# Kernel optimization log

Measured on AMD Instinct MI355X. Metric: run time of the kernel, lower is better.

## Reference

```python
import jax, jax.numpy as jnp
import numpy as np

IOU_THRESHOLDS = (0.5, 0.75)
B, N, G = 256, 4000, 50


def _iou(amin, amax, bmin, bmax):
    # broadcasted temporal IoU: anchors [N,1] vs boxes [1,G] -> [N,G]
    inter = jnp.maximum(jnp.minimum(amax, bmax) - jnp.maximum(amin, bmin), 0.0)
    union = (amax - amin) + (bmax - bmin) - inter
    return inter / union


def _greedy_tp(segments, gts, thr):
    # segments: [N,2], gts: [G,2]. Replicates AP.get_values greedy matching:
    # for each label (in order), claim the first (lowest-index) unused proposal
    # whose IoU > thr. Final used-mask == is_TP.
    ious = _iou(segments[:, 0:1], segments[:, 1:2], gts[None, :, 0], gts[None, :, 1])  # [N,G]
    pot = ious > thr
    n = segments.shape[0]

    def step(used, col):  # col: [N] bool, candidates for this label
        cand = col & ~used
        idx = jnp.argmax(cand)  # first True (argmax of bool is first max)
        used = jnp.where(jnp.any(cand), used.at[idx].set(True), used)
        return used, None

    used, _ = jax.lax.scan(step, jnp.zeros((n,), jnp.bool_), pot.T)
    return used  # [N] bool


def _ap_for_threshold(scores, segments, labels, thr):
    is_tp = jax.vmap(lambda s, g: _greedy_tp(s, g, thr))(segments, labels)  # [B,N]
    conf = scores.reshape(-1)                       # [B*N]
    tp = is_tp.reshape(-1).astype(jnp.float32)
    order = jnp.argsort(-conf)                      # sort by confidence, descending
    tp = tp[order]
    n_labels = labels.shape[0] * labels.shape[1]
    m = tp.shape[0]
    acc_tp = jnp.cumsum(tp)
    precision = acc_tp / (jnp.arange(m, dtype=jnp.float32) + 1.0)
    recall = acc_tp / jnp.float32(n_labels)
    # curve = [[1,0]] then (recall, precision) reversed; AP = sum(|dx| * cummax(y)[:-1])
    x = jnp.concatenate([jnp.ones((1,), jnp.float32), recall[::-1]])
    y = jnp.concatenate([jnp.zeros((1,), jnp.float32), precision[::-1]])
    y_max = jax.lax.cummax(y, axis=0)
    x_diff = jnp.abs(jnp.diff(x))
    return jnp.sum(x_diff * y_max[:-1])


def setup_inputs() -> dict:
    key = jax.random.key(0)
    k1, k2, k3, k4, k5 = jax.random.split(key, 5)
    scores = jax.random.uniform(k1, (B, N), dtype=jnp.float32)
    p_start = jax.random.uniform(k2, (B, N), dtype=jnp.float32) * 0.9
    p_len = jax.random.uniform(k3, (B, N), dtype=jnp.float32) * 0.1 + 0.005
    segments = jnp.stack([p_start, p_start + p_len], axis=-1)  # [B,N,2], start<end
    g_start = jax.random.uniform(k4, (B, G), dtype=jnp.float32) * 0.9
    g_len = jax.random.uniform(k5, (B, G), dtype=jnp.float32) * 0.1 + 0.005
    labels = jnp.stack([g_start, g_start + g_len], axis=-1)    # [B,G,2]
    return {"scores": scores, "segments": segments, "labels": labels}


def reference(scores, segments, labels):
    # returns AP at each IoU threshold, shape [len(IOU_THRESHOLDS)]
    return jnp.stack([_ap_for_threshold(scores, segments, labels, t) for t in IOU_THRESHOLDS])
```

## Files before the change

### kernel.cpp

```cpp
#include <hip/hip_runtime.h>


#define B_ 256
#define N_ 4000
#define G_ 50
#define M_ (B_ * N_)
#define NL_ (B_ * G_)
#define NBKT 1024
#define KP 16
#define TILE (NL_ / KP)

#define M0_ 0x1.000001p-1
#define M1_ 0x1.800001p-1

typedef unsigned long long u64;

__device__ __forceinline__ unsigned bucket_of(float c) {
    unsigned b = (unsigned)(c * 1024.0f);
    return b > (NBKT - 1) ? (NBKT - 1) : b;
}

__global__ __launch_bounds__(1024) void tp_kernel(
    const float* __restrict__ seg,
    const float* __restrict__ gts,
    const float* __restrict__ conf,
    int* __restrict__ tpIdx,
    int* __restrict__ cnt,
    unsigned short* __restrict__ pbh)
{
    const int tid  = threadIdx.x;
    const int lane = tid & 63;
    const int wv   = tid >> 6;
    const int b    = blockIdx.x;

    __shared__ float2 gtl[G_];
    __shared__ u64 cand[2][G_][64];
    __shared__ unsigned hls[NBKT];
    __shared__ int lcnt[2];

    if (tid < NBKT) hls[tid] = 0u;
    if (tid < G_) gtl[tid] = ((const float2*)gts)[b * G_ + tid];
    if (tid < 2) lcnt[tid] = 0;
    __syncthreads();

    const float* cb = conf + (size_t)b * N_;
    #pragma unroll
    for (int s = 0; s < 4; ++s) {
        int n = s * 1024 + tid;
        if (n < N_) atomicAdd(&hls[bucket_of(cb[n])], 1u);
    }

    const float2* sb = (const float2*)(seg + (size_t)b * (N_ * 2));
    float pmin[4], pmax[4], plen[4];
    #pragma unroll
    for (int s = 0; s < 4; ++s) {
        int n = s * 1024 + tid;
        if (n < N_) { float2 v = sb[n]; pmin[s] = v.x; pmax[s] = v.y; }
        else { pmin[s] = 1e9f; pmax[s] = 1e9f; }
        plen[s] = pmax[s] - pmin[s];
    }
    for (int g = 0; g < G_; ++g) {
        float2 gt = gtl[g];
        float glen = gt.y - gt.x;
        u64 m0[4], m1[4];
        #pragma unroll
        for (int s = 0; s < 4; ++s) {
            float inter = fmaxf(fminf(pmax[s], gt.y) - fmaxf(pmin[s], gt.x), 0.0f);
            float uni = plen[s] + glen - inter;
            double di = (double)inter;
            double du = (double)uni;
            m0[s] = __ballot(di > M0_ * du);
            m1[s] = __ballot(di > M1_ * du);
        }
        if (lane == 0) {
            #pragma unroll
            for (int s = 0; s < 4; ++s) {
                cand[0][g][s * 16 + wv] = m0[s];
                cand[1][g][s * 16 + wv] = m1[s];
            }
        }
    }
    __syncthreads();

    if (tid < NBKT) pbh[(size_t)b * NBKT + tid] = (unsigned short)hls[tid];

    if (wv < 2) {
        const int thr_i = wv;
        u64 used = 0ull;
        for (int g = 0; g < G_; ++g) {
            u64 c = cand[thr_i][g][lane] & ~used;
            u64 ball = __ballot(c != 0ull);
            if (ball) {
                int fl = __ffsll(ball) - 1;
                if (lane == fl) used |= (c & (0ull - c));
            }
        }
        int cpop = __popcll(used);
        if (cpop) {
            int j = atomicAdd(&lcnt[thr_i], cpop);
            u64 u = used;
            while (u) {
                int bit = __ffsll(u) - 1;
                u &= u - 1;
                tpIdx[thr_i * NL_ + b * G_ + j++] = b * N_ + lane * 64 + bit;
            }
        }
    }
    __syncthreads();
    if (tid < 2) cnt[tid * B_ + b] = lcnt[tid];
}

__global__ __launch_bounds__(256) void s1_kernel(
    unsigned short* __restrict__ pbh,
    unsigned* __restrict__ total)
{
    __shared__ unsigned sc[256];
    const int bin = blockIdx.x;
    const int b = threadIdx.x;
    unsigned v = pbh[(size_t)b * NBKT + bin];
    sc[b] = v;
    __syncthreads();
    for (int off = 1; off < 256; off <<= 1) {
        unsigned add = (b >= off) ? sc[b - off] : 0u;
        __syncthreads();
        sc[b] += add;
        __syncthreads();
    }
    pbh[(size_t)b * NBKT + bin] = (unsigned short)(sc[b] - v);
    if (b == 255) total[bin] = sc[255];
}

__global__ __launch_bounds__(1024) void s2_kernel(
    const unsigned* __restrict__ total, unsigned* __restrict__ binStart)
{
    __shared__ unsigned part[1024];
    int t = threadIdx.x;
    part[t] = total[t];
    __syncthreads();
    for (int off = 1; off < 1024; off <<= 1) {
        unsigned add = (t >= off) ? part[t - off] : 0u;
        __syncthreads();
        part[t] += add;
        __syncthreads();
    }
    binStart[t] = (t == 0) ? 0u : part[t - 1];
}

__global__ __launch_bounds__(1024) void scatter_kernel(
    const float* __restrict__ conf,
    const unsigned short* __restrict__ pbh,
    const unsigned* __restrict__ binStart,
    u64* __restrict__ sKey)
{
    __shared__ unsigned baseB[NBKT];
    __shared__ unsigned lofs[NBKT];
    const int tid = threadIdx.x;
    const int b = blockIdx.x;
    if (tid < NBKT) {
        baseB[tid] = binStart[tid] + pbh[(size_t)b * NBKT + tid];
        lofs[tid] = 0u;
    }
    __syncthreads();
    const float* cb = conf + (size_t)b * N_;
    #pragma unroll
    for (int s = 0; s < 4; ++s) {
        int n = s * 1024 + tid;
        if (n < N_) {
            float c = cb[n];
            unsigned bin = bucket_of(c);
            unsigned lo = atomicAdd(&lofs[bin], 1u);
            unsigned idx = (unsigned)(b * N_ + n);
            sKey[baseB[bin] + lo] = ((u64)__float_as_uint(c) << 32) | (u64)(0xFFFFFFFFu - idx);
        }
    }
}

__global__ __launch_bounds__(256) void rank_kernel(
    const float* __restrict__ conf,
    const int* __restrict__ tpIdx,
    const int* __restrict__ cnt,
    const unsigned* __restrict__ total,
    const unsigned* __restrict__ binStart,
    const u64* __restrict__ sKey,
    int* __restrict__ tpRank)
{
    const int lane = threadIdx.x & 63;
    const int w = (blockIdx.x << 2) | (threadIdx.x >> 6);
    if (w >= 2 * NL_) return;
    const int thr_i = w / NL_;
    const int t = w - thr_i * NL_;
    const int batch = t / G_;
    const int j = t - batch * G_;

    if (j < cnt[thr_i * B_ + batch]) {
        int e = tpIdx[thr_i * NL_ + t];
        float c = conf[e];
        u64 keyE = ((u64)__float_as_uint(c) << 32) | (u64)(0xFFFFFFFFu - (unsigned)e);
        unsigned bin = bucket_of(c);
        unsigned lo = binStart[bin], n = total[bin];
        int r = M_ - (int)lo - (int)n;
        for (unsigned base = 0; base < n; base += 64) {
            unsigned k = base + lane;
            bool pred = (k < n) && (sKey[lo + k] > keyE);
            r += (int)__popcll(__ballot(pred));
        }
        if (lane == 0) tpRank[thr_i * NL_ + t] = r;
    } else {
        if (lane == 0) tpRank[thr_i * NL_ + t] = M_ + t;
    }
}

__global__ __launch_bounds__(256) void pos1_kernel(
    const int* __restrict__ tpRank,
    int* __restrict__ pcount)
{
    __shared__ alignas(16) int tile[TILE];
    const int k = blockIdx.y, thr_i = blockIdx.z;
    const int* base = tpRank + thr_i * NL_;
    for (int i = threadIdx.x; i < TILE; i += 256)
        tile[i] = base[k * TILE + i];
    __syncthreads();

    const int t0 = blockIdx.x * 1024 + threadIdx.x;
    int r[4], c[4] = {0, 0, 0, 0};
    #pragma unroll
    for (int j = 0; j < 4; ++j) {
        int t = t0 + j * 256;
        r[j] = (t < NL_) ? base[t] : -1;
    }
    const int4* l4 = (const int4*)tile;
    #pragma unroll 4
    for (int i = 0; i < TILE / 4; ++i) {
        int4 v = l4[i];
        #pragma unroll
        for (int j = 0; j < 4; ++j)
            c[j] += (v.x < r[j]) + (v.y < r[j]) + (v.z < r[j]) + (v.w < r[j]);
    }
    #pragma unroll
    for (int j = 0; j < 4; ++j) {
        int t = t0 + j * 256;
        if (t < NL_) pcount[(thr_i * KP + k) * NL_ + t] = c[j];
    }
}

__global__ __launch_bounds__(1024) void ap_kernel(
    const int* __restrict__ tpRank,
    const int* __restrict__ pcount,
    float* __restrict__ out)
{
    const int C = 13;
    __shared__ int sr[NL_];
    __shared__ float cmax[1024];
    __shared__ double red[1024];
    int thr_i = blockIdx.x;
    int t = threadIdx.x;

    #pragma unroll
    for (int j = 0; j < C; ++j) {
        int tt = t + j * 1024;
        if (tt < NL_) {
            int p = 0;
            #pragma unroll
            for (int k = 0; k < KP; ++k)
                p += pcount[(thr_i * KP + k) * NL_ + tt];
            sr[p] = tpRank[thr_i * NL_ + tt];
        }
    }
    __syncthreads();

    float pr[C]; int rk[C];
    #pragma unroll
    for (int k = 0; k < C; ++k) {
        int i = t * C + k;
        rk[k] = (i < NL_) ? sr[i] : 0x7FFFFFFF;
        pr[k] = (rk[k] < M_) ? (float)(i + 1) / (float)(rk[k] + 1) : -1.0f;
    }
    float suf[C];
    float run = -1.0f;
    #pragma unroll
    for (int k = C - 1; k >= 0; --k) { run = fmaxf(run, pr[k]); suf[k] = run; }

    cmax[t] = run;
    __syncthreads();
    for (int off = 1; off < 1024; off <<= 1) {
        float v = cmax[t];
        float o = (t + off < 1024) ? cmax[t + off] : -1.0f;
        __syncthreads();
        cmax[t] = fmaxf(v, o);
        __syncthreads();
    }
    float follow = (t + 1 < 1024) ? cmax[t + 1] : -1.0f;

    double acc = 0.0;
    #pragma unroll
    for (int k = 0; k < C; ++k) {
        int i = t * C + k;
        if (rk[k] >= 1 && rk[k] < M_) {
            float smax = fmaxf(suf[k], follow);
            float rhi = (float)(i + 1) / 12800.0f;
            float rlo = (float)i / 12800.0f;
            acc += (double)((rhi - rlo) * smax);
        }
    }
    red[t] = acc;
    __syncthreads();
    for (int off = 512; off >= 1; off >>= 1) {
        if (t < off) red[t] += red[t + off];
        __syncthreads();
    }
    if (t == 0) out[thr_i] = (float)red[0];
}

extern "C" void kernel_launch(void* const* d_in, const int* in_sizes, int n_in,
                              void* d_out, int out_size, void* d_ws, size_t ws_size,
                              hipStream_t stream) {
    const float* scores = (const float*)d_in[0];
    const float* seg    = (const float*)d_in[1];
    const float* gts    = (const float*)d_in[2];
    float* out = (float*)d_out;

    char* p = (char*)d_ws;
    int*            cnt        = (int*)p;             p += 4096;
    int*            tpIdx      = (int*)p;             p += 2 * NL_ * 4;
    int*            tpRank     = (int*)p;             p += 2 * NL_ * 4;
    unsigned*       total      = (unsigned*)p;        p += NBKT * 4;
    unsigned*       binStart   = (unsigned*)p;        p += NBKT * 4;
    unsigned short* pbh        = (unsigned short*)p;  p += (size_t)B_ * NBKT * 2;
    u64*            sKey       = (u64*)p;             p += (size_t)M_ * 8;
    int*            pcount     = (int*)sKey;
    (void)ws_size; (void)in_sizes; (void)n_in; (void)out_size;

    tp_kernel<<<B_, 1024, 0, stream>>>(seg, gts, scores, tpIdx, cnt, pbh);
    s1_kernel<<<NBKT, 256, 0, stream>>>(pbh, total);
    s2_kernel<<<1, 1024, 0, stream>>>(total, binStart);
    scatter_kernel<<<B_, 1024, 0, stream>>>(scores, pbh, binStart, sKey);
    rank_kernel<<<(2 * NL_ + 3) / 4, 256, 0, stream>>>(scores, tpIdx, cnt,
                                                       total, binStart, sKey, tpRank);
    pos1_kernel<<<dim3(13, KP, 2), 256, 0, stream>>>(tpRank, pcount);
    ap_kernel<<<2, 1024, 0, stream>>>(tpRank, pcount, out);
}
```

Baseline: 192.2 us.

## Split greedy matching into its own kernel and enlarge confidence histogram buckets

The greedy label matching moves out of the 1024-thread tp_kernel into a separate small kernel. Candidate masks now go through a global buffer, so tp_kernel no longer keeps most of its waves idle during the serial matching loop. The confidence histogram grows from 1024 to 4096 buckets, and s2 now scans four bins per thread, so each bucket holds fewer items for the later rank step. The cost is an extra launch and global round-trip for the masks, plus larger histogram and scan work in s1, scatter and binStart.

Result: slower. 222.5 us (+15.8%).

```diff
diff --git a/kernel.cpp b/kernel.cpp
--- a/kernel.cpp
+++ b/kernel.cpp
@@ -6,7 +6,7 @@
 #define G_ 50
 #define M_ (B_ * N_)
 #define NL_ (B_ * G_)
-#define NBKT 1024
+#define NBKT 4096
 #define KP 16
 #define TILE (NL_ / KP)
 
@@ -16,7 +16,7 @@
 typedef unsigned long long u64;
 
 __device__ __forceinline__ unsigned bucket_of(float c) {
-    unsigned b = (unsigned)(c * 1024.0f);
+    unsigned b = (unsigned)(c * 4096.0f);
     return b > (NBKT - 1) ? (NBKT - 1) : b;
 }
 
@@ -24,8 +24,7 @@
     const float* __restrict__ seg,
     const float* __restrict__ gts,
     const float* __restrict__ conf,
-    int* __restrict__ tpIdx,
-    int* __restrict__ cnt,
+    u64* __restrict__ gCand,
     unsigned short* __restrict__ pbh)
 {
     const int tid  = threadIdx.x;
@@ -34,13 +33,11 @@
     const int b    = blockIdx.x;
 
     __shared__ float2 gtl[G_];
-    __shared__ u64 cand[2][G_][64];
     __shared__ unsigned hls[NBKT];
-    __shared__ int lcnt[2];
-
-    if (tid < NBKT) hls[tid] = 0u;
+
+    #pragma unroll
+    for (int k = 0; k < NBKT / 1024; ++k) hls[k * 1024 + tid] = 0u;
     if (tid < G_) gtl[tid] = ((const float2*)gts)[b * G_ + tid];
-    if (tid < 2) lcnt[tid] = 0;
     __syncthreads();
 
     const float* cb = conf + (size_t)b * N_;
@@ -59,6 +56,8 @@
         else { pmin[s] = 1e9f; pmax[s] = 1e9f; }
         plen[s] = pmax[s] - pmin[s];
     }
+    u64* c0 = gCand + ((size_t)b * G_) * 64;
+    u64* c1 = gCand + ((size_t)(B_ + b) * G_) * 64;
     for (int g = 0; g < G_; ++g) {
         float2 gt = gtl[g];
         float glen = gt.y - gt.x;
@@ -75,39 +74,54 @@
         if (lane == 0) {
             #pragma unroll
             for (int s = 0; s < 4; ++s) {
-                cand[0][g][s * 16 + wv] = m0[s];
-                cand[1][g][s * 16 + wv] = m1[s];
+                c0[g * 64 + s * 16 + wv] = m0[s];
+                c1[g * 64 + s * 16 + wv] = m1[s];
             }
         }
     }
     __syncthreads();
 
-    if (tid < NBKT) pbh[(size_t)b * NBKT + tid] = (unsigned short)hls[tid];
-
-    if (wv < 2) {
-        const int thr_i = wv;
-        u64 used = 0ull;
-        for (int g = 0; g < G_; ++g) {
-            u64 c = cand[thr_i][g][lane] & ~used;
-            u64 ball = __ballot(c != 0ull);
-            if (ball) {
-                int fl = __ffsll(ball) - 1;
-                if (lane == fl) used |= (c & (0ull - c));
-            }
-        }
-        int cpop = __popcll(used);
-        if (cpop) {
-            int j = atomicAdd(&lcnt[thr_i], cpop);
-            u64 u = used;
-            while (u) {
-                int bit = __ffsll(u) - 1;
-                u &= u - 1;
-                tpIdx[thr_i * NL_ + b * G_ + j++] = b * N_ + lane * 64 + bit;
-            }
-        }
-    }
-    __syncthreads();
-    if (tid < 2) cnt[tid * B_ + b] = lcnt[tid];
+    #pragma unroll
+    for (int k = 0; k < NBKT / 1024; ++k) {
+        int bin = k * 1024 + tid;
+        pbh[(size_t)b * NBKT + bin] = (unsigned short)hls[bin];
+    }
+}
+
+__global__ __launch_bounds__(128) void greedy_kernel(
+    const u64* __restrict__ gCand,
+    int* __restrict__ tpIdx,
+    int* __restrict__ cnt)
+{
+    const int lane = threadIdx.x & 63;
+    const int thr_i = threadIdx.x >> 6;
+    const int b = blockIdx.x;
+    const u64* cm = gCand + ((size_t)(thr_i * B_ + b) * G_) * 64;
+
+    u64 used = 0ull;
+    for (int g = 0; g < G_; ++g) {
+        u64 c = cm[g * 64 + lane] & ~used;
+        u64 ball = __ballot(c != 0ull);
+        if (ball) {
+            int fl = __ffsll(ball) - 1;
+            if (lane == fl) used |= (c & (0ull - c));
+        }
+    }
+    int cpop = __popcll(used);
+    int x = cpop;
+    #pragma unroll
+    for (int off = 1; off < 64; off <<= 1) {
+        int v = __shfl_up(x, off, 64);
+        if (lane >= off) x += v;
+    }
+    int j = x - cpop;
+    u64 u = used;
+    while (u) {
+        int bit = __ffsll(u) - 1;
+        u &= u - 1;
+        tpIdx[thr_i * NL_ + b * G_ + j++] = b * N_ + lane * 64 + bit;
+    }
+    if (lane == 63) cnt[thr_i * B_ + b] = x;
 }
 
 __global__ __launch_bounds__(256) void s1_kernel(
@@ -135,7 +149,14 @@
 {
     __shared__ unsigned part[1024];
     int t = threadIdx.x;
-    part[t] = total[t];
+    unsigned loc[4];
+    unsigned s = 0;
+    uint4 v4 = ((const uint4*)total)[t];
+    loc[0] = s; s += v4.x;
+    loc[1] = s; s += v4.y;
+    loc[2] = s; s += v4.z;
+    loc[3] = s; s += v4.w;
+    part[t] = s;
     __syncthreads();
     for (int off = 1; off < 1024; off <<= 1) {
         unsigned add = (t >= off) ? part[t - off] : 0u;
@@ -143,7 +164,9 @@
         part[t] += add;
         __syncthreads();
     }
-    binStart[t] = (t == 0) ? 0u : part[t - 1];
+    unsigned base = (t == 0) ? 0u : part[t - 1];
+    ((uint4*)binStart)[t] = make_uint4(base + loc[0], base + loc[1],
+                                       base + loc[2], base + loc[3]);
 }
 
 __global__ __launch_bounds__(1024) void scatter_kernel(
@@ -156,9 +179,11 @@
     __shared__ unsigned lofs[NBKT];
     const int tid = threadIdx.x;
     const int b = blockIdx.x;
-    if (tid < NBKT) {
-        baseB[tid] = binStart[tid] + pbh[(size_t)b * NBKT + tid];
-        lofs[tid] = 0u;
+    #pragma unroll
+    for (int k = 0; k < NBKT / 1024; ++k) {
+        int bin = k * 1024 + tid;
+        baseB[bin] = binStart[bin] + pbh[(size_t)b * NBKT + bin];
+        lofs[bin] = 0u;
     }
     __syncthreads();
     const float* cb = conf + (size_t)b * N_;
@@ -326,11 +351,13 @@
     unsigned*       total      = (unsigned*)p;        p += NBKT * 4;
     unsigned*       binStart   = (unsigned*)p;        p += NBKT * 4;
     unsigned short* pbh        = (unsigned short*)p;  p += (size_t)B_ * NBKT * 2;
+    u64*            gCand      = (u64*)p;             p += (size_t)2 * B_ * G_ * 64 * 8;
     u64*            sKey       = (u64*)p;             p += (size_t)M_ * 8;
     int*            pcount     = (int*)sKey;
     (void)ws_size; (void)in_sizes; (void)n_in; (void)out_size;
 
-    tp_kernel<<<B_, 1024, 0, stream>>>(seg, gts, scores, tpIdx, cnt, pbh);
+    tp_kernel<<<B_, 1024, 0, stream>>>(seg, gts, scores, gCand, pbh);
+    greedy_kernel<<<B_, 128, 0, stream>>>(gCand, tpIdx, cnt);
     s1_kernel<<<NBKT, 256, 0, stream>>>(pbh, total);
     s2_kernel<<<1, 1024, 0, stream>>>(total, binStart);
     scatter_kernel<<<B_, 1024, 0, stream>>>(scores, pbh, binStart, sKey);
```
